# Kernel optimization log

Hardware: AMD Instinct MI355X
Metric: run time of the kernel (lower is better)

Reference implementation:

```python
import jax, jax.numpy as jnp
import numpy as np

B, N, DIM = 2, 2048, 1024
H, DH = 16, 64
DIM_INNER = H * DH
EPS = float(jnp.finfo(jnp.float32).eps)  # torch nn.RMSNorm default eps = finfo.eps
THETA = 10000.0


def setup_inputs() -> dict:
    key = jax.random.key(0)
    ks = jax.random.split(key, 6)
    s = 0.02
    tokens = jax.random.normal(ks[0], (B, N, DIM), dtype=jnp.float32)
    w_norm = jnp.ones((DIM,), jnp.float32)                      # prenorm RMSNorm weight
    w_q = jax.random.normal(ks[1], (DIM, DIM_INNER), jnp.float32) * s
    w_k = jax.random.normal(ks[2], (DIM, 3 * DIM_INNER), jnp.float32) * s
    w_v = jax.random.normal(ks[3], (DIM, 3 * DIM_INNER), jnp.float32) * s
    w_key_norms = jnp.ones((3, DH), jnp.float32)                # 3 key RMSNorms
    w_nested_knorm = jnp.ones((DH,), jnp.float32)
    w_out = jax.random.normal(ks[4], (DIM_INNER, DIM), jnp.float32) * s
    return {"tokens": tokens, "w_norm": w_norm, "w_q": w_q, "w_k": w_k,
            "w_v": w_v, "w_key_norms": w_key_norms,
            "w_nested_knorm": w_nested_knorm, "w_out": w_out}


def rmsnorm(x, w):
    var = jnp.mean(jnp.square(x), axis=-1, keepdims=True)
    return x * jax.lax.rsqrt(var + EPS) * w


def rope(x):
    # interleaved (GPT-J style) rotary, as in rotary_embedding_torch defaults
    n, d = x.shape[-2], x.shape[-1]
    inv_freq = 1.0 / (THETA ** (jnp.arange(0, d, 2, dtype=jnp.float32) / d))
    freqs = jnp.arange(n, dtype=jnp.float32)[:, None] * inv_freq   # (n, d/2)
    cos = jnp.repeat(jnp.cos(freqs), 2, axis=-1)                   # (n, d)
    sin = jnp.repeat(jnp.sin(freqs), 2, axis=-1)
    x1, x2 = x[..., ::2], x[..., 1::2]
    x_rot = jnp.stack((-x2, x1), axis=-1).reshape(x.shape)         # rotate_half
    return x * cos + x_rot * sin


def attend(q, k, v):
    # rotate_queries_with_cached_keys with equal lengths -> plain rotary on both
    q = rope(q)
    k = rope(k)
    d = q.shape[-1]
    scores = jnp.einsum('bhqd,bhkd->bhqk', q, k) / jnp.sqrt(jnp.float32(d))
    n = scores.shape[-1]
    causal = jnp.tril(jnp.ones((n, n), dtype=bool))
    scores = jnp.where(causal, scores, -jnp.inf)
    attn = jax.nn.softmax(scores, axis=-1)
    return jnp.einsum('bhqk,bhkd->bhqd', attn, v)


def reference(tokens, w_norm, w_q, w_k, w_v, w_key_norms, w_nested_knorm, w_out):
    b, n = tokens.shape[:2]
    x = rmsnorm(tokens, w_norm)                                    # prenorm
    q = (x @ w_q).reshape(b, n, H, DH).transpose(0, 2, 1, 3)       # (b,h,n,d)
    # chunk(3, dim=-1) then split heads -> (3,b,h,n,d)
    ks = (x @ w_k).reshape(b, n, 3, H, DH).transpose(2, 0, 3, 1, 4)
    vs = (x @ w_v).reshape(b, n, 3, H, DH).transpose(2, 0, 3, 1, 4)
    ks = rmsnorm(ks, w_key_norms[:, None, None, None, :])          # per-branch key norm
    # three parallel causal attentions sharing the same queries
    nq, nk, nv = jax.vmap(attend, in_axes=(None, 0, 0))(q, ks, vs)
    nk = rmsnorm(nk, w_nested_knorm)
    out = attend(nq, nk, nv)                                       # nested attention
    out = out.transpose(0, 2, 1, 3).reshape(b, n, DIM_INNER)       # merge heads
    return out @ w_out
```

## Files before the change

kernel.cpp:

```cpp
#include <hip/hip_runtime.h>
#include <hip/hip_bf16.h>
#include <stdint.h>

typedef unsigned short u16;
typedef __attribute__((ext_vector_type(8))) short short8;
typedef __attribute__((ext_vector_type(4))) float float4v;
typedef __attribute__((ext_vector_type(4))) unsigned int uint4v;

#define B_    2
#define N_    2048
#define DIM_  1024
#define H_    16
#define DH_   64
#define DI_   1024
#define EPS_  1.1920928955078125e-07f
#define LOG2_THETA 13.287712379549449f
#define SCL_  0.18033688011112042f

__device__ __forceinline__ float bf2f(u16 u) {
    union { unsigned int i; float f; } v; v.i = ((unsigned int)u) << 16; return v.f;
}
__device__ __forceinline__ u16 f2bf(float f) {
    union { float f; unsigned int i; } v; v.f = f;
    unsigned int r = v.i + 0x7fff + ((v.i >> 16) & 1);
    return (u16)(r >> 16);
}
__device__ __forceinline__ unsigned int cvtpk(float a, float b) {
    unsigned int r;
    asm("v_cvt_pk_bf16_f32 %0, %1, %2" : "=v"(r) : "v"(a), "v"(b));
    return r;
}
__device__ __forceinline__ int perm32(int n) {
    return (n & ~31) + (((n >> 2) & 3) * 8) + (((n >> 4) & 1) * 4) + (n & 3);
}

__global__ __launch_bounds__(256) void k_pre(
    const float* __restrict__ w_q, const float* __restrict__ w_k,
    const float* __restrict__ w_v, u16* __restrict__ dstW,
    const float* __restrict__ tok, const float* __restrict__ w_norm,
    u16* __restrict__ xn) {
    int bx = blockIdx.x;
    int t = threadIdx.x;
    __shared__ float tile[32][33];
    __shared__ float red[4];
    if (bx < 7168) {
        int c0 = (bx % 224) * 32, k0 = (bx / 224) * 32;
        const float* src; int sN, sc0;
        if (c0 < 1024)      { src = w_q; sN = 1024; sc0 = c0; }
        else if (c0 < 4096) { src = w_k; sN = 3072; sc0 = c0 - 1024; }
        else                { src = w_v; sN = 3072; sc0 = c0 - 4096; }
        int tx = t & 31, ty = t >> 5;
#pragma unroll
        for (int i = 0; i < 4; ++i)
            tile[ty + 8 * i][tx] = src[(size_t)(k0 + ty + 8 * i) * sN + sc0 + tx];
        __syncthreads();
#pragma unroll
        for (int i = 0; i < 4; ++i)
            dstW[(size_t)(c0 + ty + 8 * i) * 1024 + k0 + tx] = f2bf(tile[tx][ty + 8 * i]);
    } else {
        int row = bx - 7168;
        const float* tr = tok + (size_t)row * DIM_ + t * 4;
        float4v v = *(const float4v*)tr;
        float ss = v[0] * v[0] + v[1] * v[1] + v[2] * v[2] + v[3] * v[3];
#pragma unroll
        for (int o = 32; o; o >>= 1) ss += __shfl_xor(ss, o, 64);
        if ((t & 63) == 0) red[t >> 6] = ss;
        __syncthreads();
        ss = red[0] + red[1] + red[2] + red[3];
        float rs = rsqrtf(ss * (1.0f / DIM_) + EPS_);
        const float* wp = w_norm + t * 4;
        uint2 pk;
        pk.x = cvtpk(v[0] * rs * wp[0], v[1] * rs * wp[1]);
        pk.y = cvtpk(v[2] * rs * wp[2], v[3] * rs * wp[3]);
        *(uint2*)(xn + (size_t)row * DIM_ + t * 4) = pk;
    }
}

__global__ __launch_bounds__(256) void k_transpose(
    const float* __restrict__ src, u16* __restrict__ dst, int K, int N) {
    __shared__ float tile[32][33];
    int n0 = blockIdx.x * 32, k0 = blockIdx.y * 32;
    int tx = threadIdx.x, ty = threadIdx.y;
#pragma unroll
    for (int i = 0; i < 4; ++i)
        tile[ty + 8 * i][tx] = src[(size_t)(k0 + ty + 8 * i) * N + n0 + tx];
    __syncthreads();
#pragma unroll
    for (int i = 0; i < 4; ++i)
        dst[(size_t)(n0 + ty + 8 * i) * K + k0 + tx] = f2bf(tile[tx][ty + 8 * i]);
}

__global__ __launch_bounds__(256) void k_post1(
    u16* __restrict__ QKVB, u16* __restrict__ Vt, const float* __restrict__ w) {
    int bx = blockIdx.x;
    int t = threadIdx.x;
    __shared__ u16 tile[64][72];
    if (bx < 3072) {
        int y = bx >> 5;
        int s = y >> 5;
        int b = (y >> 4) & 1;
        int h = y & 15;
        int n0 = (bx & 31) * 64;
#pragma unroll
        for (int i = 0; i < 2; ++i) {
            int idx = i * 256 + t;
            int row = idx >> 3, c = idx & 7;
            uint4v v = *(const uint4v*)(QKVB + ((size_t)(b * N_) + n0 + row) * 7168
                                            + 4096 + s * 1024 + h * 64 + c * 8);
            *(uint4v*)&tile[row][c * 8] = v;
        }
        __syncthreads();
        u16* out = Vt + (size_t)y * 64 * N_;
#pragma unroll
        for (int i = 0; i < 2; ++i) {
            int idx = i * 256 + t;
            int dh = idx >> 3, og = idx & 7;
            u16 vals[8];
#pragma unroll
            for (int j = 0; j < 8; ++j) {
                int m = og * 8 + j;
                int nn = (m & 32) + (m & 3) + ((m >> 3) & 3) * 4 + ((m >> 2) & 1) * 16;
                vals[j] = tile[nn][dh];
            }
            *(uint4v*)(out + (size_t)dh * N_ + n0 + og * 8) = *(const uint4v*)vals;
        }
    } else {
        int wid = (bx - 3072) * 4 + (t >> 6);
        int lane = t & 63;
        int r8 = lane >> 3, e8 = lane & 7;
        int hg = wid & 1;
        int s = (wid >> 1) % 3;
        int row = wid / 6;
        int n = row & (N_ - 1);
        int h = hg * 8 + r8;
        u16* p = QKVB + (size_t)row * 7168 + 1024 + s * 1024 + h * 64 + e8 * 8;
        uint4v v = *(const uint4v*)p;
        float x[8];
#pragma unroll
        for (int j = 0; j < 8; ++j) x[j] = bf2f(((const u16*)&v)[j]);
        float ss = 0.f;
#pragma unroll
        for (int j = 0; j < 8; ++j) ss += x[j] * x[j];
        ss += __shfl_xor(ss, 1, 64);
        ss += __shfl_xor(ss, 2, 64);
        ss += __shfl_xor(ss, 4, 64);
        float rs = rsqrtf(ss * (1.0f / 64.0f) + EPS_);
        const float* ws = w + s * 64 + e8 * 8;
        uint4v pk;
#pragma unroll
        for (int tp = 0; tp < 4; ++tp) {
            int d0 = e8 * 8 + 2 * tp;
            float xn0 = x[2 * tp] * rs * ws[2 * tp];
            float xn1 = x[2 * tp + 1] * rs * ws[2 * tp + 1];
            float inv = exp2f(-(float)d0 * (LOG2_THETA / 64.0f));
            float fr = (float)n * inv;
            float sv, cv;
            __sincosf(fr, &sv, &cv);
            pk[tp] = cvtpk(xn0 * cv - xn1 * sv, xn1 * cv + xn0 * sv);
        }
        *(uint4v*)p = pk;
    }
}

template <bool OUT_F32>
__global__ __launch_bounds__(256) void k_gemm_bt(
    const u16* __restrict__ A, const u16* __restrict__ Bt, void* __restrict__ Cv,
    int K, int Ncols) {
    int nwg = gridDim.x;
    int chunk = nwg >> 3;
    int wg = (blockIdx.x & 7) * chunk + (blockIdx.x >> 3);
    int m0 = (wg & 31) * 128, n0 = (wg >> 5) * 128;
    __shared__ u16 As[2][128 * 32];
    __shared__ u16 Bs[2][128 * 32];
    int t = threadIdx.x;
    int w = t >> 6, lane = t & 63, ln = lane & 15, quad = lane >> 4;
    int wm = w & 1, wn = w >> 1;
    float4v acc[4][4] = {};

    const u16* gA[2];
    const u16* gB[2];
    int ldsoff[2];
#pragma unroll
    for (int i = 0; i < 2; ++i) {
        int idx = i * 256 + t;
        int row = idx >> 2, kb = idx & 3;
        int csrc = (kb ^ ((row >> 1) & 3)) * 8;
        gA[i] = A + (size_t)(m0 + row) * K + csrc;
        gB[i] = Bt + (size_t)(n0 + row) * K + csrc;
        ldsoff[i] = idx * 8;
    }

    auto stage = [&](int buf) {
#pragma unroll
        for (int i = 0; i < 2; ++i) {
            __builtin_amdgcn_global_load_lds(
                (const __attribute__((address_space(1))) void*)gA[i],
                (__attribute__((address_space(3))) void*)(As[buf] + ldsoff[i]), 16, 0, 0);
            __builtin_amdgcn_global_load_lds(
                (const __attribute__((address_space(1))) void*)gB[i],
                (__attribute__((address_space(3))) void*)(Bs[buf] + ldsoff[i]), 16, 0, 0);
            gA[i] += 32; gB[i] += 32;
        }
    };

    int nk = K >> 5;
    stage(0);
    int rchunk = (quad ^ ((ln >> 1) & 3)) * 8;

    for (int kt = 0; kt < nk; ++kt) {
        asm volatile("s_waitcnt vmcnt(0)" ::: "memory");
        __syncthreads();
        if (kt + 1 < nk) stage((kt + 1) & 1);
        int buf = kt & 1;
        short8 af[4], bfr[4];
#pragma unroll
        for (int mt = 0; mt < 4; ++mt)
            af[mt] = *(const short8*)(As[buf] + (wm * 64 + mt * 16 + ln) * 32 + rchunk);
#pragma unroll
        for (int nt = 0; nt < 4; ++nt)
            bfr[nt] = *(const short8*)(Bs[buf] + (wn * 64 + nt * 16 + ln) * 32 + rchunk);
#pragma unroll
        for (int mt = 0; mt < 4; ++mt)
#pragma unroll
            for (int nt = 0; nt < 4; ++nt)
                acc[mt][nt] = __builtin_amdgcn_mfma_f32_16x16x32_bf16(
                    af[mt], bfr[nt], acc[mt][nt], 0, 0, 0);
    }
#pragma unroll
    for (int mt = 0; mt < 4; ++mt)
#pragma unroll
        for (int nt = 0; nt < 4; ++nt)
#pragma unroll
            for (int r = 0; r < 4; ++r) {
                int row = m0 + wm * 64 + mt * 16 + quad * 4 + r;
                int col = n0 + wn * 64 + nt * 16 + ln;
                if (OUT_F32)
                    ((float*)Cv)[(size_t)row * Ncols + col] = acc[mt][nt][r];
                else
                    ((u16*)Cv)[(size_t)row * Ncols + col] = f2bf(acc[mt][nt][r]);
            }
}

template <int WIN>
__global__ __launch_bounds__(256, WIN == 1 ? 3 : 2) void k_flash(
    const u16* __restrict__ Q, int q_stride,
    const u16* __restrict__ K, const u16* __restrict__ Vt,
    u16* __restrict__ O, u16* __restrict__ Ot,
    int kv_stride, int set_off, size_t o_set_stride,
    const float* __restrict__ wnk) {
    constexpr bool PRIO = (WIN == 2);
    int bh = blockIdx.x;
    int qt = gridDim.y - 1 - blockIdx.y;
    int s = blockIdx.z;
    int b = bh >> 4, h = bh & 15;
    int t = threadIdx.x;
    int w = t >> 6, lane = t & 63, ln = lane & 15, quad = lane >> 4;
    int lnx = ln & 7;
    int q0 = qt * 128;
    int qw = q0 + w * 32;

    const u16* Qb  = Q + ((size_t)b * N_) * q_stride + h * 64;
    const u16* Kb  = K + ((size_t)b * N_) * kv_stride + (size_t)s * set_off + h * 64;
    const u16* Vtb = Vt + (size_t)((s * B_ + b) * H_ + h) * (64 * (size_t)N_);

    __shared__ u16 Ks[2][WIN][64][64];
    __shared__ u16 Vs[2][WIN][64][64];

    short8 ones;
#pragma unroll
    for (int j = 0; j < 8; ++j) ((u16*)&ones)[j] = 0x3F80;

    short8 qf[2][2];
    float mrow[2];
    float4v accO[2][4] = {};
    float4v accL[2] = {};
#pragma unroll
    for (int g = 0; g < 2; ++g) {
        int qg = qw + g * 16;
        int tokn = qg + ln;
        short8 raw[2];
#pragma unroll
        for (int f = 0; f < 2; ++f)
            raw[f] = *(const short8*)(Qb + (size_t)tokn * q_stride + f * 32 + quad * 8);
        float qn = 0.f;
#pragma unroll
        for (int f = 0; f < 2; ++f)
#pragma unroll
            for (int j = 0; j < 8; ++j) {
                float v = bf2f(((const u16*)&raw[f])[j]);
                qn += v * v;
            }
        qn += __shfl_xor(qn, 16, 64);
        qn += __shfl_xor(qn, 32, 64);
        mrow[g] = sqrtf(qn) * (8.0f * SCL_) * 1.03f + 1e-6f;
#pragma unroll
        for (int f = 0; f < 2; ++f) {
            u16 out8[8];
            int dbase = f * 32 + quad * 8;
#pragma unroll
            for (int tp = 0; tp < 4; ++tp) {
                int d = dbase + 2 * tp;
                float inv = exp2f((float)d * (-LOG2_THETA / 64.0f));
                float fr = (float)tokn * inv;
                float sv, cv;
                __sincosf(fr, &sv, &cv);
                float x0 = bf2f(((const u16*)&raw[f])[2 * tp]);
                float x1 = bf2f(((const u16*)&raw[f])[2 * tp + 1]);
                out8[2 * tp]     = f2bf((x0 * cv - x1 * sv) * SCL_);
                out8[2 * tp + 1] = f2bf((x1 * cv + x0 * sv) * SCL_);
            }
            qf[g][f] = *(const short8*)out8;
        }
    }

    int ntb = 2 * qt + 2;
    int nwin = ntb / WIN;

    const u16* kP[2];
    const u16* vP[2];
    int ldsoff[2];
    u16* ldsKbase = &Ks[0][0][0][0];
    u16* ldsVbase = &Vs[0][0][0][0];
#pragma unroll
    for (int i = 0; i < 2; ++i) {
        int idx = i * 256 + t;
        int row = idx >> 3, c = idx & 7;
        int csrc = ((c ^ (row & 7)) * 8);
        kP[i] = Kb + (size_t)row * kv_stride + csrc;
        vP[i] = Vtb + (size_t)row * N_ + csrc;
        ldsoff[i] = row * 64 + c * 8;
    }
    int kAdvance = 64 * kv_stride;

    auto stage = [&](int buf) {
#pragma unroll
        for (int sub = 0; sub < WIN; ++sub) {
            int toff = (buf * WIN + sub) * (64 * 64);
#pragma unroll
            for (int i = 0; i < 2; ++i) {
                __builtin_amdgcn_global_load_lds(
                    (const __attribute__((address_space(1))) void*)kP[i],
                    (__attribute__((address_space(3))) void*)(ldsKbase + toff + ldsoff[i]), 16, 0, 0);
                __builtin_amdgcn_global_load_lds(
                    (const __attribute__((address_space(1))) void*)vP[i],
                    (__attribute__((address_space(3))) void*)(ldsVbase + toff + ldsoff[i]), 16, 0, 0);
                kP[i] += kAdvance;
                vP[i] += 64;
            }
        }
    };

    auto compute = [&](int buf, int sub, int k0) {
        short8 kf[4][2];
#pragma unroll
        for (int kt = 0; kt < 4; ++kt) {
            const u16* krow = &Ks[buf][sub][kt * 16 + ln][0];
            kf[kt][0] = *(const short8*)(krow + ((quad ^ lnx) * 8));
            kf[kt][1] = *(const short8*)(krow + (((4 + quad) ^ lnx) * 8));
        }
        short8 pb[2][2];
#pragma unroll
        for (int g = 0; g < 2; ++g) {
            int qg = qw + g * 16;
            float4v st[4];
            if (PRIO) __builtin_amdgcn_s_setprio(1);
#pragma unroll
            for (int kt = 0; kt < 4; ++kt) {
                float4v sa = {-mrow[g], -mrow[g], -mrow[g], -mrow[g]};
                sa = __builtin_amdgcn_mfma_f32_16x16x32_bf16(kf[kt][0], qf[g][0], sa, 0, 0, 0);
                sa = __builtin_amdgcn_mfma_f32_16x16x32_bf16(kf[kt][1], qf[g][1], sa, 0, 0, 0);
                st[kt] = sa;
            }
            if (PRIO) __builtin_amdgcn_s_setprio(0);
            if (k0 + 63 <= qg) {
#pragma unroll
                for (int c = 0; c < 2; ++c) {
                    uint4v pk;
#pragma unroll
                    for (int kt2 = 0; kt2 < 2; ++kt2) {
                        pk[kt2 * 2 + 0] = cvtpk(exp2f(st[c * 2 + kt2][0]),
                                                exp2f(st[c * 2 + kt2][1]));
                        pk[kt2 * 2 + 1] = cvtpk(exp2f(st[c * 2 + kt2][2]),
                                                exp2f(st[c * 2 + kt2][3]));
                    }
                    pb[g][c] = *(short8*)&pk;
                }
            } else {
                int qr = qg + ln;
#pragma unroll
                for (int c = 0; c < 2; ++c) {
                    uint4v pk;
#pragma unroll
                    for (int kt2 = 0; kt2 < 2; ++kt2) {
                        int kt = c * 2 + kt2;
                        float e[4];
#pragma unroll
                        for (int r = 0; r < 4; ++r) {
                            int kg = k0 + kt * 16 + quad * 4 + r;
                            float arg = (kg <= qr) ? st[kt][r] : -1e30f;
                            e[r] = exp2f(arg);
                        }
                        pk[kt2 * 2 + 0] = cvtpk(e[0], e[1]);
                        pk[kt2 * 2 + 1] = cvtpk(e[2], e[3]);
                    }
                    pb[g][c] = *(short8*)&pk;
                }
            }
        }
        if (PRIO) __builtin_amdgcn_s_setprio(1);
#pragma unroll
        for (int dc = 0; dc < 4; ++dc) {
            const u16* vrow = &Vs[buf][sub][dc * 16 + ln][0];
            short8 vf0 = *(const short8*)(vrow + ((quad ^ lnx) * 8));
            short8 vf1 = *(const short8*)(vrow + (((4 + quad) ^ lnx) * 8));
#pragma unroll
            for (int g = 0; g < 2; ++g) {
                accO[g][dc] = __builtin_amdgcn_mfma_f32_16x16x32_bf16(vf0, pb[g][0], accO[g][dc], 0, 0, 0);
                accO[g][dc] = __builtin_amdgcn_mfma_f32_16x16x32_bf16(vf1, pb[g][1], accO[g][dc], 0, 0, 0);
            }
        }
#pragma unroll
        for (int g = 0; g < 2; ++g) {
            accL[g] = __builtin_amdgcn_mfma_f32_16x16x32_bf16(ones, pb[g][0], accL[g], 0, 0, 0);
            accL[g] = __builtin_amdgcn_mfma_f32_16x16x32_bf16(ones, pb[g][1], accL[g], 0, 0, 0);
        }
        if (PRIO) __builtin_amdgcn_s_setprio(0);
    };

    stage(0);

    for (int wv = 0; wv < nwin; ++wv) {
        asm volatile("s_waitcnt vmcnt(0)" ::: "memory");
        __syncthreads();
        if (wv + 1 < nwin) stage((wv + 1) & 1);
        int buf = wv & 1;
        int k0 = wv * (WIN * 64);
        if (k0 > qw + 31) continue;
        compute(buf, 0, k0);
        if (WIN == 2 && k0 + 64 <= qw + 31)
            compute(buf, 1, k0 + 64);
    }

#pragma unroll
    for (int g = 0; g < 2; ++g) {
        float rinv = 1.0f / accL[g][0];
        int qg = qw + g * 16;
        int qr = qg + ln;
        if (s == 2) {
            u16* Otb = Ot + (size_t)(b * H_ + h) * (64 * (size_t)N_);
            int pos = perm32(qr & (N_ - 1)) + (qr & ~(N_ - 1));
#pragma unroll
            for (int dc = 0; dc < 4; ++dc)
#pragma unroll
                for (int r = 0; r < 4; ++r)
                    Otb[(size_t)(dc * 16 + quad * 4 + r) * N_ + pos] =
                        f2bf(accO[g][dc][r] * rinv);
        } else if (wnk && s == 1) {
            u16* Ob = O + o_set_stride + ((size_t)b * N_) * DI_ + h * 64;
            float o[4][4];
            float ss = 0.f;
#pragma unroll
            for (int dc = 0; dc < 4; ++dc)
#pragma unroll
                for (int r = 0; r < 4; ++r) {
                    float x = accO[g][dc][r] * rinv;
                    o[dc][r] = x;
                    ss += x * x;
                }
            ss += __shfl_xor(ss, 16, 64);
            ss += __shfl_xor(ss, 32, 64);
            float rs2 = rsqrtf(ss * (1.0f / 64.0f) + EPS_);
#pragma unroll
            for (int dc = 0; dc < 4; ++dc) {
                uint2 pk;
#pragma unroll
                for (int rp = 0; rp < 2; ++rp) {
                    int d0 = dc * 16 + quad * 4 + 2 * rp;
                    float x0 = o[dc][2 * rp]     * rs2 * wnk[d0];
                    float x1 = o[dc][2 * rp + 1] * rs2 * wnk[d0 + 1];
                    float inv = exp2f(-(float)d0 * (LOG2_THETA / 64.0f));
                    float fr = (float)qr * inv;
                    float sv, cv;
                    __sincosf(fr, &sv, &cv);
                    unsigned int u = cvtpk(x0 * cv - x1 * sv, x1 * cv + x0 * sv);
                    if (rp == 0) pk.x = u; else pk.y = u;
                }
                *(uint2*)(Ob + (size_t)qr * DI_ + dc * 16 + quad * 4) = pk;
            }
        } else {
            u16* Ob = O + (size_t)s * o_set_stride + ((size_t)b * N_) * DI_ + h * 64;
#pragma unroll
            for (int dc = 0; dc < 4; ++dc) {
                uint2 pk;
                pk.x = cvtpk(accO[g][dc][0] * rinv, accO[g][dc][1] * rinv);
                pk.y = cvtpk(accO[g][dc][2] * rinv, accO[g][dc][3] * rinv);
                *(uint2*)(Ob + (size_t)qr * DI_ + dc * 16 + quad * 4) = pk;
            }
        }
    }
}

extern "C" void kernel_launch(void* const* d_in, const int* in_sizes, int n_in,
                              void* d_out, int out_size, void* d_ws, size_t ws_size,
                              hipStream_t stream) {
    const float* tok     = (const float*)d_in[0];
    const float* w_norm  = (const float*)d_in[1];
    const float* w_q     = (const float*)d_in[2];
    const float* w_k     = (const float*)d_in[3];
    const float* w_v     = (const float*)d_in[4];
    const float* w_keyn  = (const float*)d_in[5];
    const float* w_nestk = (const float*)d_in[6];
    const float* w_o     = (const float*)d_in[7];

    char* ws = (char*)d_ws;
    const size_t MB = 1024 * 1024;
    u16* QKVB  = (u16*)(ws + 0 * MB);
    u16* VtB   = (u16*)(ws + 56 * MB);
    u16* NQKV  = (u16*)(ws + 80 * MB);
    u16* WQKVT = (u16*)(ws + 80 * MB);
    u16* NVt   = (u16*)(ws + 96 * MB);
    u16* XN    = (u16*)(ws + 96 * MB);
    u16* OUT2  = (u16*)(ws + 104 * MB);
    u16* WOT   = (u16*)(ws + 80 * MB);

    const size_t SET = (size_t)B_ * N_ * DI_;

    k_pre<<<7168 + 4096, 256, 0, stream>>>(w_q, w_k, w_v, WQKVT, tok, w_norm, XN);

    k_gemm_bt<false><<<1792, 256, 0, stream>>>(XN, WQKVT, QKVB, 1024, 7168);

    k_post1<<<3072 + 6144, 256, 0, stream>>>(QKVB, VtB, w_keyn);

    k_flash<1><<<dim3(B_ * H_, N_ / 128, 3), 256, 0, stream>>>(
        QKVB, 7168, QKVB + 1024, VtB, NQKV, NVt, 7168, 1024, SET, w_nestk);

    k_flash<2><<<dim3(B_ * H_, N_ / 128, 1), 256, 0, stream>>>(
        NQKV, 1024, NQKV + SET, NVt, OUT2, NVt , 1024, 0, 0, nullptr);

    k_transpose<<<dim3(32, 32), dim3(32, 8), 0, stream>>>(w_o, WOT, 1024, 1024);
    k_gemm_bt<true><<<256, 256, 0, stream>>>(OUT2, WOT, (float*)d_out, 1024, 1024);
}
```

Measured before the change: 356.8 us.

## Pair complementary causal query tiles per block in nested flash attention

The flash kernel can now loop over two query tiles per block, pairing tile qt with NQT-1-qt so every block does the same amount of causal work. The nested attention launch halves its grid in y to use this mode. The goal is to remove the causal load imbalance and tail effect from a small grid (512 blocks). The cost is fewer blocks and two sequential phases with an extra barrier, which lowers parallelism across the CUs.

```diff
diff --git a/kernel.cpp b/kernel.cpp
--- a/kernel.cpp
+++ b/kernel.cpp
@@ -250,14 +250,11 @@
     const float* __restrict__ wnk) {
     constexpr bool PRIO = (WIN == 2);
     int bh = blockIdx.x;
-    int qt = gridDim.y - 1 - blockIdx.y;
     int s = blockIdx.z;
     int b = bh >> 4, h = bh & 15;
     int t = threadIdx.x;
     int w = t >> 6, lane = t & 63, ln = lane & 15, quad = lane >> 4;
     int lnx = ln & 7;
-    int q0 = qt * 128;
-    int qw = q0 + w * 32;
 
     const u16* Qb  = Q + ((size_t)b * N_) * q_stride + h * 64;
     const u16* Kb  = K + ((size_t)b * N_) * kv_stride + (size_t)s * set_off + h * 64;
@@ -270,64 +267,17 @@
 #pragma unroll
     for (int j = 0; j < 8; ++j) ((u16*)&ones)[j] = 0x3F80;
 
-    short8 qf[2][2];
-    float mrow[2];
-    float4v accO[2][4] = {};
-    float4v accL[2] = {};
-#pragma unroll
-    for (int g = 0; g < 2; ++g) {
-        int qg = qw + g * 16;
-        int tokn = qg + ln;
-        short8 raw[2];
-#pragma unroll
-        for (int f = 0; f < 2; ++f)
-            raw[f] = *(const short8*)(Qb + (size_t)tokn * q_stride + f * 32 + quad * 8);
-        float qn = 0.f;
-#pragma unroll
-        for (int f = 0; f < 2; ++f)
-#pragma unroll
-            for (int j = 0; j < 8; ++j) {
-                float v = bf2f(((const u16*)&raw[f])[j]);
-                qn += v * v;
-            }
-        qn += __shfl_xor(qn, 16, 64);
-        qn += __shfl_xor(qn, 32, 64);
-        mrow[g] = sqrtf(qn) * (8.0f * SCL_) * 1.03f + 1e-6f;
-#pragma unroll
-        for (int f = 0; f < 2; ++f) {
-            u16 out8[8];
-            int dbase = f * 32 + quad * 8;
-#pragma unroll
-            for (int tp = 0; tp < 4; ++tp) {
-                int d = dbase + 2 * tp;
-                float inv = exp2f((float)d * (-LOG2_THETA / 64.0f));
-                float fr = (float)tokn * inv;
-                float sv, cv;
-                __sincosf(fr, &sv, &cv);
-                float x0 = bf2f(((const u16*)&raw[f])[2 * tp]);
-                float x1 = bf2f(((const u16*)&raw[f])[2 * tp + 1]);
-                out8[2 * tp]     = f2bf((x0 * cv - x1 * sv) * SCL_);
-                out8[2 * tp + 1] = f2bf((x1 * cv + x0 * sv) * SCL_);
-            }
-            qf[g][f] = *(const short8*)out8;
-        }
-    }
-
-    int ntb = 2 * qt + 2;
-    int nwin = ntb / WIN;
-
     const u16* kP[2];
     const u16* vP[2];
-    int ldsoff[2];
+    int rowi[2], csrci[2], ldsoff[2];
     u16* ldsKbase = &Ks[0][0][0][0];
     u16* ldsVbase = &Vs[0][0][0][0];
 #pragma unroll
     for (int i = 0; i < 2; ++i) {
         int idx = i * 256 + t;
         int row = idx >> 3, c = idx & 7;
-        int csrc = ((c ^ (row & 7)) * 8);
-        kP[i] = Kb + (size_t)row * kv_stride + csrc;
-        vP[i] = Vtb + (size_t)row * N_ + csrc;
+        rowi[i] = row;
+        csrci[i] = (c ^ (row & 7)) * 8;
         ldsoff[i] = row * 64 + c * 8;
     }
     int kAdvance = 64 * kv_stride;
@@ -350,151 +300,213 @@
         }
     };
 
-    auto compute = [&](int buf, int sub, int k0) {
-        short8 kf[4][2];
-#pragma unroll
-        for (int kt = 0; kt < 4; ++kt) {
-            const u16* krow = &Ks[buf][sub][kt * 16 + ln][0];
-            kf[kt][0] = *(const short8*)(krow + ((quad ^ lnx) * 8));
-            kf[kt][1] = *(const short8*)(krow + (((4 + quad) ^ lnx) * 8));
-        }
-        short8 pb[2][2];
+    const int NQT = N_ / 128;
+    int nhalf = (gridDim.y * 2 == NQT) ? 2 : 1;
+
+    for (int half = 0; half < nhalf; ++half) {
+        int qt = half ? blockIdx.y : (NQT - 1 - blockIdx.y);
+        int q0 = qt * 128;
+        int qw = q0 + w * 32;
+
+        if (half) __syncthreads();
+
+        short8 qf[2][2];
+        float mrow[2];
+        float4v accO[2][4] = {};
+        float4v accL[2] = {};
 #pragma unroll
         for (int g = 0; g < 2; ++g) {
             int qg = qw + g * 16;
-            float4v st[4];
-            if (PRIO) __builtin_amdgcn_s_setprio(1);
-#pragma unroll
-            for (int kt = 0; kt < 4; ++kt) {
-                float4v sa = {-mrow[g], -mrow[g], -mrow[g], -mrow[g]};
-                sa = __builtin_amdgcn_mfma_f32_16x16x32_bf16(kf[kt][0], qf[g][0], sa, 0, 0, 0);
-                sa = __builtin_amdgcn_mfma_f32_16x16x32_bf16(kf[kt][1], qf[g][1], sa, 0, 0, 0);
-                st[kt] = sa;
-            }
-            if (PRIO) __builtin_amdgcn_s_setprio(0);
-            if (k0 + 63 <= qg) {
-#pragma unroll
-                for (int c = 0; c < 2; ++c) {
-                    uint4v pk;
-#pragma unroll
-                    for (int kt2 = 0; kt2 < 2; ++kt2) {
-                        pk[kt2 * 2 + 0] = cvtpk(exp2f(st[c * 2 + kt2][0]),
-                                                exp2f(st[c * 2 + kt2][1]));
-                        pk[kt2 * 2 + 1] = cvtpk(exp2f(st[c * 2 + kt2][2]),
-                                                exp2f(st[c * 2 + kt2][3]));
-                    }
-                    pb[g][c] = *(short8*)&pk;
-                }
-            } else {
-                int qr = qg + ln;
-#pragma unroll
-                for (int c = 0; c < 2; ++c) {
-                    uint4v pk;
-#pragma unroll
-                    for (int kt2 = 0; kt2 < 2; ++kt2) {
-                        int kt = c * 2 + kt2;
-                        float e[4];
-#pragma unroll
-                        for (int r = 0; r < 4; ++r) {
-                            int kg = k0 + kt * 16 + quad * 4 + r;
-                            float arg = (kg <= qr) ? st[kt][r] : -1e30f;
-                            e[r] = exp2f(arg);
-                        }
-                        pk[kt2 * 2 + 0] = cvtpk(e[0], e[1]);
-                        pk[kt2 * 2 + 1] = cvtpk(e[2], e[3]);
-                    }
-                    pb[g][c] = *(short8*)&pk;
-                }
-            }
-        }
-        if (PRIO) __builtin_amdgcn_s_setprio(1);
-#pragma unroll
-        for (int dc = 0; dc < 4; ++dc) {
-            const u16* vrow = &Vs[buf][sub][dc * 16 + ln][0];
-            short8 vf0 = *(const short8*)(vrow + ((quad ^ lnx) * 8));
-            short8 vf1 = *(const short8*)(vrow + (((4 + quad) ^ lnx) * 8));
-#pragma unroll
-            for (int g = 0; g < 2; ++g) {
-                accO[g][dc] = __builtin_amdgcn_mfma_f32_16x16x32_bf16(vf0, pb[g][0], accO[g][dc], 0, 0, 0);
-                accO[g][dc] = __builtin_amdgcn_mfma_f32_16x16x32_bf16(vf1, pb[g][1], accO[g][dc], 0, 0, 0);
-            }
-        }
-#pragma unroll
-        for (int g = 0; g < 2; ++g) {
-            accL[g] = __builtin_amdgcn_mfma_f32_16x16x32_bf16(ones, pb[g][0], accL[g], 0, 0, 0);
-            accL[g] = __builtin_amdgcn_mfma_f32_16x16x32_bf16(ones, pb[g][1], accL[g], 0, 0, 0);
-        }
-        if (PRIO) __builtin_amdgcn_s_setprio(0);
-    };
-
-    stage(0);
-
-    for (int wv = 0; wv < nwin; ++wv) {
-        asm volatile("s_waitcnt vmcnt(0)" ::: "memory");
-        __syncthreads();
-        if (wv + 1 < nwin) stage((wv + 1) & 1);
-        int buf = wv & 1;
-        int k0 = wv * (WIN * 64);
-        if (k0 > qw + 31) continue;
-        compute(buf, 0, k0);
-        if (WIN == 2 && k0 + 64 <= qw + 31)
-            compute(buf, 1, k0 + 64);
-    }
-
-#pragma unroll
-    for (int g = 0; g < 2; ++g) {
-        float rinv = 1.0f / accL[g][0];
-        int qg = qw + g * 16;
-        int qr = qg + ln;
-        if (s == 2) {
-            u16* Otb = Ot + (size_t)(b * H_ + h) * (64 * (size_t)N_);
-            int pos = perm32(qr & (N_ - 1)) + (qr & ~(N_ - 1));
-#pragma unroll
-            for (int dc = 0; dc < 4; ++dc)
-#pragma unroll
-                for (int r = 0; r < 4; ++r)
-                    Otb[(size_t)(dc * 16 + quad * 4 + r) * N_ + pos] =
-                        f2bf(accO[g][dc][r] * rinv);
-        } else if (wnk && s == 1) {
-            u16* Ob = O + o_set_stride + ((size_t)b * N_) * DI_ + h * 64;
-            float o[4][4];
-            float ss = 0.f;
-#pragma unroll
-            for (int dc = 0; dc < 4; ++dc)
-#pragma unroll
-                for (int r = 0; r < 4; ++r) {
-                    float x = accO[g][dc][r] * rinv;
-                    o[dc][r] = x;
-                    ss += x * x;
-                }
-            ss += __shfl_xor(ss, 16, 64);
-            ss += __shfl_xor(ss, 32, 64);
-            float rs2 = rsqrtf(ss * (1.0f / 64.0f) + EPS_);
-#pragma unroll
-            for (int dc = 0; dc < 4; ++dc) {
-                uint2 pk;
-#pragma unroll
-                for (int rp = 0; rp < 2; ++rp) {
-                    int d0 = dc * 16 + quad * 4 + 2 * rp;
-                    float x0 = o[dc][2 * rp]     * rs2 * wnk[d0];
-                    float x1 = o[dc][2 * rp + 1] * rs2 * wnk[d0 + 1];
-                    float inv = exp2f(-(float)d0 * (LOG2_THETA / 64.0f));
-                    float fr = (float)qr * inv;
+            int tokn = qg + ln;
+            short8 raw[2];
+#pragma unroll
+            for (int f = 0; f < 2; ++f)
+                raw[f] = *(const short8*)(Qb + (size_t)tokn * q_stride + f * 32 + quad * 8);
+            float qn = 0.f;
+#pragma unroll
+            for (int f = 0; f < 2; ++f)
+#pragma unroll
+                for (int j = 0; j < 8; ++j) {
+                    float v = bf2f(((const u16*)&raw[f])[j]);
+                    qn += v * v;
+                }
+            qn += __shfl_xor(qn, 16, 64);
+            qn += __shfl_xor(qn, 32, 64);
+            mrow[g] = sqrtf(qn) * (8.0f * SCL_) * 1.03f + 1e-6f;
+#pragma unroll
+            for (int f = 0; f < 2; ++f) {
+                u16 out8[8];
+                int dbase = f * 32 + quad * 8;
+#pragma unroll
+                for (int tp = 0; tp < 4; ++tp) {
+                    int d = dbase + 2 * tp;
+                    float inv = exp2f((float)d * (-LOG2_THETA / 64.0f));
+                    float fr = (float)tokn * inv;
                     float sv, cv;
                     __sincosf(fr, &sv, &cv);
-                    unsigned int u = cvtpk(x0 * cv - x1 * sv, x1 * cv + x0 * sv);
-                    if (rp == 0) pk.x = u; else pk.y = u;
-                }
-                *(uint2*)(Ob + (size_t)qr * DI_ + dc * 16 + quad * 4) = pk;
+                    float x0 = bf2f(((const u16*)&raw[f])[2 * tp]);
+                    float x1 = bf2f(((const u16*)&raw[f])[2 * tp + 1]);
+                    out8[2 * tp]     = f2bf((x0 * cv - x1 * sv) * SCL_);
+                    out8[2 * tp + 1] = f2bf((x1 * cv + x0 * sv) * SCL_);
+                }
+                qf[g][f] = *(const short8*)out8;
             }
-        } else {
-            u16* Ob = O + (size_t)s * o_set_stride + ((size_t)b * N_) * DI_ + h * 64;
-#pragma unroll
-            for (int dc = 0; dc < 4; ++dc) {
-                uint2 pk;
-                pk.x = cvtpk(accO[g][dc][0] * rinv, accO[g][dc][1] * rinv);
-                pk.y = cvtpk(accO[g][dc][2] * rinv, accO[g][dc][3] * rinv);
-                *(uint2*)(Ob + (size_t)qr * DI_ + dc * 16 + quad * 4) = pk;
+        }
+
+#pragma unroll
+        for (int i = 0; i < 2; ++i) {
+            kP[i] = Kb + (size_t)rowi[i] * kv_stride + csrci[i];
+            vP[i] = Vtb + (size_t)rowi[i] * N_ + csrci[i];
+        }
+
+        int ntb = 2 * qt + 2;
+        int nwin = ntb / WIN;
+        stage(0);
+
+        for (int wv = 0; wv < nwin; ++wv) {
+            asm volatile("s_waitcnt vmcnt(0)" ::: "memory");
+            __syncthreads();
+            if (wv + 1 < nwin) stage((wv + 1) & 1);
+            int buf = wv & 1;
+            int k0 = wv * (WIN * 64);
+            if (k0 > qw + 31) continue;
+
+#pragma unroll
+            for (int sub = 0; sub < WIN; ++sub) {
+                int kk0 = k0 + sub * 64;
+                if (sub == 1 && kk0 > qw + 31) break;
+                short8 kf[4][2];
+#pragma unroll
+                for (int kt = 0; kt < 4; ++kt) {
+                    const u16* krow = &Ks[buf][sub][kt * 16 + ln][0];
+                    kf[kt][0] = *(const short8*)(krow + ((quad ^ lnx) * 8));
+                    kf[kt][1] = *(const short8*)(krow + (((4 + quad) ^ lnx) * 8));
+                }
+                short8 pb[2][2];
+#pragma unroll
+                for (int g = 0; g < 2; ++g) {
+                    int qg = qw + g * 16;
+                    float4v st[4];
+                    if (PRIO) __builtin_amdgcn_s_setprio(1);
+#pragma unroll
+                    for (int kt = 0; kt < 4; ++kt) {
+                        float4v sa = {-mrow[g], -mrow[g], -mrow[g], -mrow[g]};
+                        sa = __builtin_amdgcn_mfma_f32_16x16x32_bf16(kf[kt][0], qf[g][0], sa, 0, 0, 0);
+                        sa = __builtin_amdgcn_mfma_f32_16x16x32_bf16(kf[kt][1], qf[g][1], sa, 0, 0, 0);
+                        st[kt] = sa;
+                    }
+                    if (PRIO) __builtin_amdgcn_s_setprio(0);
+                    if (kk0 + 63 <= qg) {
+#pragma unroll
+                        for (int c = 0; c < 2; ++c) {
+                            uint4v pk;
+#pragma unroll
+                            for (int kt2 = 0; kt2 < 2; ++kt2) {
+                                pk[kt2 * 2 + 0] = cvtpk(exp2f(st[c * 2 + kt2][0]),
+                                                        exp2f(st[c * 2 + kt2][1]));
+                                pk[kt2 * 2 + 1] = cvtpk(exp2f(st[c * 2 + kt2][2]),
+                                                        exp2f(st[c * 2 + kt2][3]));
+                            }
+                            pb[g][c] = *(short8*)&pk;
+                        }
+                    } else {
+                        int qr = qg + ln;
+#pragma unroll
+                        for (int c = 0; c < 2; ++c) {
+                            uint4v pk;
+#pragma unroll
+                            for (int kt2 = 0; kt2 < 2; ++kt2) {
+                                int kt = c * 2 + kt2;
+                                float e[4];
+#pragma unroll
+                                for (int r = 0; r < 4; ++r) {
+                                    int kg = kk0 + kt * 16 + quad * 4 + r;
+                                    float arg = (kg <= qr) ? st[kt][r] : -1e30f;
+                                    e[r] = exp2f(arg);
+                                }
+                                pk[kt2 * 2 + 0] = cvtpk(e[0], e[1]);
+                                pk[kt2 * 2 + 1] = cvtpk(e[2], e[3]);
+                            }
+                            pb[g][c] = *(short8*)&pk;
+                        }
+                    }
+                }
+                if (PRIO) __builtin_amdgcn_s_setprio(1);
+#pragma unroll
+                for (int dc = 0; dc < 4; ++dc) {
+                    const u16* vrow = &Vs[buf][sub][dc * 16 + ln][0];
+                    short8 vf0 = *(const short8*)(vrow + ((quad ^ lnx) * 8));
+                    short8 vf1 = *(const short8*)(vrow + (((4 + quad) ^ lnx) * 8));
+#pragma unroll
+                    for (int g = 0; g < 2; ++g) {
+                        accO[g][dc] = __builtin_amdgcn_mfma_f32_16x16x32_bf16(vf0, pb[g][0], accO[g][dc], 0, 0, 0);
+                        accO[g][dc] = __builtin_amdgcn_mfma_f32_16x16x32_bf16(vf1, pb[g][1], accO[g][dc], 0, 0, 0);
+                    }
+                }
+#pragma unroll
+                for (int g = 0; g < 2; ++g) {
+                    accL[g] = __builtin_amdgcn_mfma_f32_16x16x32_bf16(ones, pb[g][0], accL[g], 0, 0, 0);
+                    accL[g] = __builtin_amdgcn_mfma_f32_16x16x32_bf16(ones, pb[g][1], accL[g], 0, 0, 0);
+                }
+                if (PRIO) __builtin_amdgcn_s_setprio(0);
+            }
+        }
+
+#pragma unroll
+        for (int g = 0; g < 2; ++g) {
+            float rinv = 1.0f / accL[g][0];
+            int qg = qw + g * 16;
+            int qr = qg + ln;
+            if (s == 2) {
+                u16* Otb = Ot + (size_t)(b * H_ + h) * (64 * (size_t)N_);
+                int pos = perm32(qr & (N_ - 1)) + (qr & ~(N_ - 1));
+#pragma unroll
+                for (int dc = 0; dc < 4; ++dc)
+#pragma unroll
+                    for (int r = 0; r < 4; ++r)
+                        Otb[(size_t)(dc * 16 + quad * 4 + r) * N_ + pos] =
+                            f2bf(accO[g][dc][r] * rinv);
+            } else if (wnk && s == 1) {
+                u16* Ob = O + o_set_stride + ((size_t)b * N_) * DI_ + h * 64;
+                float o[4][4];
+                float ss = 0.f;
+#pragma unroll
+                for (int dc = 0; dc < 4; ++dc)
+#pragma unroll
+                    for (int r = 0; r < 4; ++r) {
+                        float x = accO[g][dc][r] * rinv;
+                        o[dc][r] = x;
+                        ss += x * x;
+                    }
+                ss += __shfl_xor(ss, 16, 64);
+                ss += __shfl_xor(ss, 32, 64);
+                float rs2 = rsqrtf(ss * (1.0f / 64.0f) + EPS_);
+#pragma unroll
+                for (int dc = 0; dc < 4; ++dc) {
+                    uint2 pk;
+#pragma unroll
+                    for (int rp = 0; rp < 2; ++rp) {
+                        int d0 = dc * 16 + quad * 4 + 2 * rp;
+                        float x0 = o[dc][2 * rp]     * rs2 * wnk[d0];
+                        float x1 = o[dc][2 * rp + 1] * rs2 * wnk[d0 + 1];
+                        float inv = exp2f(-(float)d0 * (LOG2_THETA / 64.0f));
+                        float fr = (float)qr * inv;
+                        float sv, cv;
+                        __sincosf(fr, &sv, &cv);
+                        unsigned int u = cvtpk(x0 * cv - x1 * sv, x1 * cv + x0 * sv);
+                        if (rp == 0) pk.x = u; else pk.y = u;
+                    }
+                    *(uint2*)(Ob + (size_t)qr * DI_ + dc * 16 + quad * 4) = pk;
+                }
+            } else {
+                u16* Ob = O + (size_t)s * o_set_stride + ((size_t)b * N_) * DI_ + h * 64;
+#pragma unroll
+                for (int dc = 0; dc < 4; ++dc) {
+                    uint2 pk;
+                    pk.x = cvtpk(accO[g][dc][0] * rinv, accO[g][dc][1] * rinv);
+                    pk.y = cvtpk(accO[g][dc][2] * rinv, accO[g][dc][3] * rinv);
+                    *(uint2*)(Ob + (size_t)qr * DI_ + dc * 16 + quad * 4) = pk;
+                }
             }
         }
     }
@@ -534,7 +546,7 @@
     k_flash<1><<<dim3(B_ * H_, N_ / 128, 3), 256, 0, stream>>>(
         QKVB, 7168, QKVB + 1024, VtB, NQKV, NVt, 7168, 1024, SET, w_nestk);
 
-    k_flash<2><<<dim3(B_ * H_, N_ / 128, 1), 256, 0, stream>>>(
+    k_flash<2><<<dim3(B_ * H_, N_ / 256, 1), 256, 0, stream>>>(
         NQKV, 1024, NQKV + SET, NVt, OUT2, NVt , 1024, 0, 0, nullptr);
 
     k_transpose<<<dim3(32, 32), dim3(32, 8), 0, stream>>>(w_o, WOT, 1024, 1024);
```

New measurement: 385.4 us. 8.0% more time.
